# Optimization experiments

Hardware: AMD Instinct MI355X
Metric: run time of the kernel (lower is better)

The kernel has to match this reference:

```python
import jax, jax.numpy as jnp
import numpy as np

B, S, D = 2, 2048, 1024
H, KV, HD = 16, 4, 64
F, E, K = 2816, 8, 2
EPS = 1e-6

def setup_inputs() -> dict:
    key = jax.random.key(0)
    ks = jax.random.split(key, 9)
    def rn(k, shape, std=0.02):
        return jax.random.normal(k, shape, dtype=jnp.float32) * std
    inv_freq = 1.0 / (10000.0 ** (jnp.arange(0, HD, 2, dtype=jnp.float32) / HD))
    freqs = jnp.arange(S, dtype=jnp.float32)[:, None] * inv_freq[None, :]
    emb = jnp.concatenate([freqs, freqs], axis=-1)  # [S, HD]
    return {
        'hidden_states': rn(ks[0], (B, S, D), 1.0),
        'ln1_w': jnp.ones((D,), jnp.float32),
        'ln2_w': jnp.ones((D,), jnp.float32),
        'q_w': rn(ks[1], (H * HD, D)), 'q_b': jnp.zeros((H * HD,), jnp.float32),
        'k_w': rn(ks[2], (KV * HD, D)), 'k_b': jnp.zeros((KV * HD,), jnp.float32),
        'v_w': rn(ks[3], (KV * HD, D)), 'v_b': jnp.zeros((KV * HD,), jnp.float32),
        'o_w': rn(ks[4], (D, H * HD)),
        'router_w': rn(ks[5], (E, D), 0.01),
        'gate_w': rn(ks[6], (E, D, F)),
        'up_w': rn(ks[7], (E, D, F)),
        'down_w': rn(ks[8], (E, F, D)),
        'cos': jnp.cos(emb), 'sin': jnp.sin(emb),
    }

def _rmsnorm(x, w):
    v = jnp.mean(jnp.square(x.astype(jnp.float32)), axis=-1, keepdims=True)
    return (x.astype(jnp.float32) * jax.lax.rsqrt(v + EPS)).astype(x.dtype) * w

def _rotate_half(x):
    h = x.shape[-1] // 2
    return jnp.concatenate([-x[..., h:], x[..., :h]], axis=-1)

def reference(hidden_states, ln1_w, ln2_w, q_w, q_b, k_w, k_b, v_w, v_b, o_w, router_w, gate_w, up_w, down_w, cos, sin):
    # --- attention block (RMSNorm -> Qwen2Attention with RoPE+GQA -> residual) ---
    residual = hidden_states
    h = _rmsnorm(hidden_states, ln1_w)
    q = (h @ q_w.T + q_b).reshape(B, S, H, HD).transpose(0, 2, 1, 3)   # [B,H,S,HD]
    k = (h @ k_w.T + k_b).reshape(B, S, KV, HD).transpose(0, 2, 1, 3)  # [B,KV,S,HD]
    v = (h @ v_w.T + v_b).reshape(B, S, KV, HD).transpose(0, 2, 1, 3)
    c = cos[None, None]; s = sin[None, None]
    q = q * c + _rotate_half(q) * s
    k = k * c + _rotate_half(k) * s
    rep = H // KV
    k = jnp.repeat(k, rep, axis=1)
    v = jnp.repeat(v, rep, axis=1)
    scores = jnp.einsum('bhqd,bhkd->bhqk', q, k) / jnp.sqrt(jnp.float32(HD))
    causal = jnp.tril(jnp.ones((S, S), dtype=bool))
    scores = jnp.where(causal[None, None], scores, jnp.finfo(scores.dtype).min)
    attn = jax.nn.softmax(scores, axis=-1)
    ctx = jnp.einsum('bhqk,bhkd->bhqd', attn, v).transpose(0, 2, 1, 3).reshape(B, S, H * HD)
    x = ctx @ o_w.T + residual
    # --- MoE block (RMSNorm -> router -> expert SwiGLU MLPs -> combine -> residual) ---
    residual = x
    t = _rmsnorm(x, ln2_w).reshape(-1, D)  # [T, D], T = B*S
    logits = t @ router_w.T                # [T, E]
    probs = jax.nn.softmax(logits, axis=-1)
    topk_p, topk_i = jax.lax.top_k(probs, K)
    topk_p = topk_p / jnp.sum(topk_p, axis=-1, keepdims=True)
    # dispatch/combine weights [T,E]: vectorized form of the per-token scatter loop
    w = jnp.sum(jax.nn.one_hot(topk_i, E, dtype=t.dtype) * topk_p[..., None], axis=1)
    aux_loss = jnp.mean(E * jnp.square(jnp.mean(probs, axis=0)))
    out = jnp.zeros_like(t)
    for e in range(E):  # fixed small expert loop
        he = jax.nn.silu(t @ gate_w[e]) * (t @ up_w[e])
        out = out + (he @ down_w[e]) * w[:, e:e + 1]
    x = out.reshape(B, S, D) + residual
    return (x, aux_loss)
```

## Files before the change

### kernel.cpp

```cpp
#include <hip/hip_runtime.h>
#include <hip/hip_bf16.h>

#define DEVI __device__ __forceinline__

typedef float f32x4 __attribute__((ext_vector_type(4)));
typedef _Float16 f16x8 __attribute__((ext_vector_type(8)));
typedef short s16x8 __attribute__((ext_vector_type(8)));
typedef unsigned int u32;

constexpr int Bc = 2, Sc = 2048, Dc = 1024, Hc = 16, KVc = 4, HDc = 64, Fc = 2816, Ec = 8;
constexpr int Tc = Bc * Sc;
constexpr int QKVN = Hc * HDc + 2 * KVc * HDc;
constexpr int CAP = Tc * 2 + Ec * 128;
constexpr float LO_SCALE = 1024.0f;
constexpr float LO_INV = 1.0f / 1024.0f;

DEVI f32x4 mfma16(f16x8 a, f16x8 b, f32x4 c) {
    return __builtin_amdgcn_mfma_f32_16x16x32_f16(a, b, c, 0, 0, 0);
}
DEVI f32x4 mfma16(s16x8 a, s16x8 b, f32x4 c) {
    return __builtin_amdgcn_mfma_f32_16x16x32_bf16(a, b, c, 0, 0, 0);
}

DEVI void gll16(const void *g, void *l) {
    __builtin_amdgcn_global_load_lds(
        (const __attribute__((address_space(1))) u32 *)g,
        (__attribute__((address_space(3))) u32 *)l, 16, 0, 0);
}

DEVI u32 pack2(_Float16 a, _Float16 b) {
    union { _Float16 h[2]; u32 u; } t;
    t.h[0] = a; t.h[1] = b;
    return t.u;
}

template <int N> DEVI void wait_vm() {
    if constexpr (N == 0) asm volatile("s_waitcnt vmcnt(0)" ::: "memory");
    else if constexpr (N == 4) asm volatile("s_waitcnt vmcnt(4)" ::: "memory");
    else if constexpr (N == 6) asm volatile("s_waitcnt vmcnt(6)" ::: "memory");
    else if constexpr (N == 8) asm volatile("s_waitcnt vmcnt(8)" ::: "memory");
}

template <typename VT> struct FragT;
template <> struct FragT<_Float16> { using type = f16x8; };
template <> struct FragT<__hip_bfloat16> { using type = s16x8; };

struct GemmP {
    const void *Ah, *Al;
    const void *Bh, *Bl, *Bh2;
    long lda, ldb, bExp, K;
    const int *poff, *gidx;
    const float *bias, *resid, *bw;
    float *outF, *outF2;
    __hip_bfloat16 *outBF;
    _Float16 *rQh, *rQl, *rKh, *rKl;
    long ldc;
    int epi;
};

template <typename VT, bool SPLIT, bool GATHER, bool GU, int BN, bool XSWZ = false>
__global__ __launch_bounds__(256, SPLIT ? 3 : ((GU && BN == 128) ? 2 : 4)) void gemm_k(GemmP p) {
    constexpr int BM = 128;
    constexpr int NJ = BN / 32;
    constexpr bool HAS2 = SPLIT || GU;
    constexpr int ACH = SPLIT ? 1024 : 512;
    constexpr int BCH = BN * 4;
    constexpr int NB = HAS2 ? 2 : 1;
    constexpr int TOT = ACH + NB * BCH;
    constexpr int NCH = TOT / 256;
    constexpr int BUFVT = TOT * 8;
    constexpr int AOFF2 = 4096;
    constexpr int BOFF = ACH * 8;
    constexpr int B2OFF = (ACH + BCH) * 8;
    __shared__ __align__(16) VT s[2][BUFVT];
    const int tid = threadIdx.x, lane = tid & 63;
    const int wid = tid >> 6, wm = wid >> 1, wn = wid & 1;
    const int x = lane & 15, hi = lane >> 4;
    int mb = (int)blockIdx.x;
    if constexpr (XSWZ) mb = (mb & 7) * ((int)gridDim.x >> 3) + (mb >> 3);
    long m0 = (long)mb * BM, n0 = (long)blockIdx.y * BN;
    int e = 0;
    if (p.poff) {
        int tot = p.poff[Ec];
        if (m0 >= tot) return;
        while (m0 >= p.poff[e + 1]) ++e;
    }

    const VT *gs[NCH];
    int chd[NCH];
#pragma unroll
    for (int i = 0; i < NCH; ++i) {
        int ch = tid + i * 256;
        chd[i] = ch;
        if (ch < ACH) {
            int slab = ch >> 9, local = ch & 511;
            int r = local >> 2, c = local & 3;
            int cs = c ^ ((r >> 1) & 3);
            long ar = m0 + r;
            if (GATHER) ar = p.gidx[ar];
            const VT *mat = (SPLIT && slab == 1) ? (const VT *)p.Al : (const VT *)p.Ah;
            gs[i] = mat + ar * p.lda + cs * 8;
        } else {
            int idx = ch - ACH;
            int which = idx / BCH, local = idx % BCH;
            int r = local >> 2, c = local & 3;
            int cs = c ^ ((r >> 1) & 3);
            const VT *bmat = (which == 0) ? (const VT *)p.Bh
                           : (SPLIT ? (const VT *)p.Bl : (const VT *)p.Bh2);
            gs[i] = bmat + (long)e * p.bExp + (n0 + r) * p.ldb + cs * 8;
        }
    }

    f32x4 acc[4][NJ];
    f32x4 acc2[HAS2 ? 4 : 1][HAS2 ? NJ : 1];
#pragma unroll
    for (int i = 0; i < 4; ++i)
#pragma unroll
        for (int j = 0; j < NJ; ++j) {
            acc[i][j] = (f32x4){0.f, 0.f, 0.f, 0.f};
            if constexpr (HAS2) acc2[i][j] = (f32x4){0.f, 0.f, 0.f, 0.f};
        }

    using F8 = typename FragT<VT>::type;
    const int KT = (int)(p.K / 32);
    auto stageTo = [&](int kt, int b) {
#pragma unroll
        for (int i = 0; i < NCH; ++i)
            gll16(gs[i] + (long)kt * 32, &s[b][(size_t)chd[i] * 8]);
    };

    stageTo(0, 0);
    if (KT > 1) stageTo(1, 1);

    for (int kt = 0; kt < KT; ++kt) {
        if (kt + 1 < KT) wait_vm<NCH>();
        else wait_vm<0>();
        __builtin_amdgcn_sched_barrier(0);
        __builtin_amdgcn_s_barrier();
        __builtin_amdgcn_sched_barrier(0);
        const int cur = kt & 1;

        F8 afh[4], afl[SPLIT ? 4 : 1];
#pragma unroll
        for (int mi = 0; mi < 4; ++mi) {
            int ar = wm * 64 + mi * 16 + x;
            int ad = (ar * 4 + (hi ^ ((ar >> 1) & 3))) * 8;
            afh[mi] = *(const F8 *)&s[cur][ad];
            if constexpr (SPLIT) afl[mi] = *(const F8 *)&s[cur][AOFF2 + ad];
        }
        __builtin_amdgcn_s_setprio(1);
#pragma unroll
        for (int nj = 0; nj < NJ; ++nj) {
            int br = wn * (BN / 2) + nj * 16 + x;
            int bd = (br * 4 + (hi ^ ((br >> 1) & 3))) * 8;
            F8 bfh = *(const F8 *)&s[cur][BOFF + bd];
            F8 bf2;
            if constexpr (HAS2) bf2 = *(const F8 *)&s[cur][B2OFF + bd];
#pragma unroll
            for (int mi = 0; mi < 4; ++mi) {
                acc[mi][nj] = mfma16(afh[mi], bfh, acc[mi][nj]);
                if constexpr (SPLIT) {
                    acc2[mi][nj] = mfma16(afh[mi], bf2, acc2[mi][nj]);
                    acc2[mi][nj] = mfma16(afl[mi], bfh, acc2[mi][nj]);
                }
                if constexpr (GU) acc2[mi][nj] = mfma16(afh[mi], bf2, acc2[mi][nj]);
            }
        }
        __builtin_amdgcn_s_setprio(0);

        asm volatile("s_waitcnt lgkmcnt(0)" ::: "memory");
        __builtin_amdgcn_sched_barrier(0);
        __builtin_amdgcn_s_barrier();
        __builtin_amdgcn_sched_barrier(0);
        if (kt + 2 < KT) stageTo(kt + 2, cur);
    }

    if (SPLIT && p.epi == 6) {
        float *sEpi = (float *)&s[0][0];
#pragma unroll
        for (int mi = 0; mi < 4; ++mi)
#pragma unroll
            for (int nj = 0; nj < NJ; ++nj)
#pragma unroll
                for (int r = 0; r < 4; ++r) {
                    int rl = wm * 64 + mi * 16 + hi * 4 + r;
                    int cl = wn * (BN / 2) + nj * 16 + x;
                    float v = fmaf(acc2[mi][nj][r], LO_INV, acc[mi][nj][r]) + p.bias[n0 + cl];
                    sEpi[rl * 64 + cl] = v;
                }
        __syncthreads();
        const bool isV = (n0 >= 1280);
        const bool isK = (n0 >= 1024) && !isV;
#pragma unroll
        for (int mi = 0; mi < 4; ++mi)
#pragma unroll
            for (int nj = 0; nj < NJ; ++nj)
#pragma unroll
                for (int r = 0; r < 4; ++r) {
                    int rl = wm * 64 + mi * 16 + hi * 4 + r;
                    int cl = wn * (BN / 2) + nj * 16 + x;
                    long row = m0 + rl;
                    float xv = sEpi[rl * 64 + cl];
                    if (isV) {
                        p.outF[row * 256 + (n0 - 1280) + cl] = xv;
                    } else {
                        int spos = (int)(row & (Sc - 1));
                        float xp = sEpi[rl * 64 + (cl ^ 32)];
                        float cs = p.resid[spos * 64 + cl];
                        float sn = p.bw[spos * 64 + cl];
                        float o = xv * cs + ((cl < 32) ? -xp : xp) * sn;
                        _Float16 hv = (_Float16)o;
                        _Float16 lo = (_Float16)((o - (float)hv) * LO_SCALE);
                        if (isK) {
                            long off = row * 256 + (n0 - 1024) + cl;
                            p.rKh[off] = hv; p.rKl[off] = lo;
                        } else {
                            long off = row * 1024 + n0 + cl;
                            p.rQh[off] = hv; p.rQl[off] = lo;
                        }
                    }
                }
        return;
    }

#pragma unroll
    for (int mi = 0; mi < 4; ++mi)
#pragma unroll
        for (int nj = 0; nj < NJ; ++nj)
#pragma unroll
            for (int r = 0; r < 4; ++r) {
                long row = m0 + wm * 64 + mi * 16 + hi * 4 + r;
                long col = n0 + wn * (BN / 2) + nj * 16 + x;
                float v = acc[mi][nj][r];
                if constexpr (GU) {
                    float u = acc2[mi][nj][r];
                    float he = v / (1.f + __expf(-v)) * u;
                    p.outBF[row * p.ldc + col] = __float2bfloat16(he);
                } else {
                    if constexpr (SPLIT) v = fmaf(acc2[mi][nj][r], LO_INV, v);
                    switch (p.epi) {
                    case 0: p.outF[row * p.ldc + col] = v + p.bias[col]; break;
                    case 2: {
                        float o = v + p.resid[row * p.ldc + col];
                        p.outF[row * p.ldc + col] = o;
                        p.outF2[row * p.ldc + col] = o;
                    } break;
                    case 5:
                        p.outF[row * p.ldc + col] = v * p.bw[row];
                        break;
                    }
                }
            }
}

__global__ __launch_bounds__(256) void combine_k(const float *__restrict__ scat,
        const int *__restrict__ tok_slot, float *__restrict__ out) {
    const long tok = blockIdx.x;
    const int c = threadIdx.x * 4;
    const long s0 = tok_slot[tok * 2], s1 = tok_slot[tok * 2 + 1];
    f32x4 a = *(const f32x4 *)(scat + s0 * Dc + c);
    f32x4 b = *(const f32x4 *)(scat + s1 * Dc + c);
    f32x4 o = *(const f32x4 *)(out + tok * Dc + c);
#pragma unroll
    for (int j = 0; j < 4; ++j) o[j] += a[j] + b[j];
    *(f32x4 *)(out + tok * Dc + c) = o;
}

__global__ __launch_bounds__(128, 2) void attn_k(
    const _Float16 *__restrict__ qh, const _Float16 *__restrict__ ql,
    const _Float16 *__restrict__ kh, const _Float16 *__restrict__ kl,
    const _Float16 *__restrict__ vTh, const _Float16 *__restrict__ vTl,
    _Float16 *__restrict__ ctxh, _Float16 *__restrict__ ctxl) {
    __shared__ __align__(16) _Float16 kbuf[2][2][32 * 64];
    __shared__ __align__(16) _Float16 vbuf[2][2][64 * 32];
    const int tid = threadIdx.x, lane = tid & 63, wid = tid >> 6;
    const int x = lane & 15, hi = lane >> 4;
    const int pairI = blockIdx.x;
    const int bh = blockIdx.y;
    const int b = bh >> 4, h = bh & 15, kvh = h >> 2;
    const long kRow0 = (long)b * Sc * 256;
    const long vRow0 = (long)(b * 4 + kvh) * 64 * (long)Sc;

    auto stage = [&](int kt, int bufI) {
        if (wid == 0) {
#pragma unroll
            for (int ss = 0; ss < 2; ++ss) {
                const _Float16 *src = ss ? kl : kh;
#pragma unroll
                for (int i = 0; i < 4; ++i) {
                    int kv = 8 * i + (lane >> 3);
                    int cd = (lane & 7) ^ (kv & 7);
                    const _Float16 *g = src + kRow0 + ((long)kt * 32 + kv) * 256 + kvh * 64 + cd * 8;
                    gll16(g, &kbuf[bufI][ss][i * 512]);
                }
            }
        } else {
#pragma unroll
            for (int ss = 0; ss < 2; ++ss) {
                const _Float16 *src = ss ? vTl : vTh;
#pragma unroll
                for (int i = 0; i < 4; ++i) {
                    int d = 16 * i + (lane >> 2);
                    int ckv = (lane & 3) ^ ((d >> 1) & 3);
                    const _Float16 *g = src + vRow0 + (long)d * Sc + (long)kt * 32 + ckv * 8;
                    gll16(g, &vbuf[bufI][ss][i * 512]);
                }
            }
        }
    };

    for (int seg = 0; seg < 2; ++seg) {
        const int qt = seg ? (63 - pairI) : pairI;
        const int q0 = qt * 32;
        const long qtokW = (long)b * Sc + q0 + wid * 16;

        f16x8 qfh[2], qfl[2];
#pragma unroll
        for (int ks = 0; ks < 2; ++ks) {
            long off = (qtokW + x) * (long)Dc + h * 64 + ks * 32 + hi * 8;
            qfh[ks] = *(const f16x8 *)(qh + off);
            qfl[ks] = *(const f16x8 *)(ql + off);
        }
        asm volatile("s_waitcnt vmcnt(0)" ::: "memory");
        __builtin_amdgcn_sched_barrier(0);

        f32x4 o1[4], o2[4];
        float mrow = -3.0e38f, lrow = 0.f;
#pragma unroll
        for (int dj = 0; dj < 4; ++dj) {
            o1[dj] = (f32x4){0.f, 0.f, 0.f, 0.f};
            o2[dj] = (f32x4){0.f, 0.f, 0.f, 0.f};
        }

        const int NT = qt + 1;

        stage(0, 0);
        stage(1, 1);

        for (int kt = 0; kt < NT; ++kt) {
            if (kt + 1 < NT) asm volatile("s_waitcnt vmcnt(8)" ::: "memory");
            else asm volatile("s_waitcnt vmcnt(0)" ::: "memory");
            __builtin_amdgcn_sched_barrier(0);
            __builtin_amdgcn_s_barrier();
            __builtin_amdgcn_sched_barrier(0);
            const int cur = kt & 1;

            f32x4 s1[2], s2[2];
#pragma unroll
            for (int kvs = 0; kvs < 2; ++kvs) {
                s1[kvs] = (f32x4){0.f, 0.f, 0.f, 0.f};
                s2[kvs] = (f32x4){0.f, 0.f, 0.f, 0.f};
            }
            __builtin_amdgcn_s_setprio(1);
#pragma unroll
            for (int ks = 0; ks < 2; ++ks)
#pragma unroll
                for (int kvs = 0; kvs < 2; ++kvs) {
                    int row = kvs * 16 + x;
                    int addr = row * 64 + (((ks * 4 + hi) ^ (row & 7)) << 3);
                    f16x8 kfh = *(const f16x8 *)&kbuf[cur][0][addr];
                    f16x8 kfl = *(const f16x8 *)&kbuf[cur][1][addr];
                    s1[kvs] = mfma16(kfh, qfh[ks], s1[kvs]);
                    s2[kvs] = mfma16(kfl, qfh[ks], s2[kvs]);
                    s2[kvs] = mfma16(kfh, qfl[ks], s2[kvs]);
                }
            __builtin_amdgcn_s_setprio(0);

            const bool diag = (kt == NT - 1);
            const int qpos = q0 + wid * 16 + x;
            float sv[2][4];
#pragma unroll
            for (int kvs = 0; kvs < 2; ++kvs)
#pragma unroll
                for (int r = 0; r < 4; ++r) {
                    float v = fmaf(s2[kvs][r], LO_INV, s1[kvs][r]) * 0.125f;
                    if (diag) {
                        int kvpos = kt * 32 + kvs * 16 + 4 * hi + r;
                        if (kvpos > qpos) v = -3.0e38f;
                    }
                    sv[kvs][r] = v;
                }
            float mx = sv[0][0];
#pragma unroll
            for (int kvs = 0; kvs < 2; ++kvs)
#pragma unroll
                for (int r = 0; r < 4; ++r) mx = fmaxf(mx, sv[kvs][r]);
            mx = fmaxf(mx, __shfl_xor(mx, 16));
            mx = fmaxf(mx, __shfl_xor(mx, 32));
            if (!__all(mx - mrow <= 8.0f)) {
                float mnew = fmaxf(mrow, mx);
                float scl = __expf(mrow - mnew);
                mrow = mnew;
                lrow *= scl;
                float sclr[4];
#pragma unroll
                for (int r = 0; r < 4; ++r) sclr[r] = __shfl(scl, 4 * hi + r);
#pragma unroll
                for (int dj = 0; dj < 4; ++dj)
#pragma unroll
                    for (int r = 0; r < 4; ++r) {
                        o1[dj][r] *= sclr[r];
                        o2[dj][r] *= sclr[r];
                    }
            }
            float pv[2][4];
            float ls = 0.f;
#pragma unroll
            for (int kvs = 0; kvs < 2; ++kvs)
#pragma unroll
                for (int r = 0; r < 4; ++r) {
                    pv[kvs][r] = __expf(sv[kvs][r] - mrow);
                    ls += pv[kvs][r];
                }
            ls += __shfl_xor(ls, 16);
            ls += __shfl_xor(ls, 32);
            lrow += ls;
            u32 Bh0[2], Bh1[2], Bl0[2], Bl1[2];
#pragma unroll
            for (int pr = 0; pr < 2; ++pr) {
                _Float16 a0 = (_Float16)pv[0][2 * pr], a1 = (_Float16)pv[0][2 * pr + 1];
                _Float16 b0 = (_Float16)pv[1][2 * pr], b1 = (_Float16)pv[1][2 * pr + 1];
                Bh0[pr] = pack2(a0, a1);
                Bh1[pr] = pack2(b0, b1);
                _Float16 la0 = (_Float16)((pv[0][2 * pr] - (float)a0) * LO_SCALE);
                _Float16 la1 = (_Float16)((pv[0][2 * pr + 1] - (float)a1) * LO_SCALE);
                _Float16 lb0 = (_Float16)((pv[1][2 * pr] - (float)b0) * LO_SCALE);
                _Float16 lb1 = (_Float16)((pv[1][2 * pr + 1] - (float)b1) * LO_SCALE);
                Bl0[pr] = pack2(la0, la1);
                Bl1[pr] = pack2(lb0, lb1);
            }
            const int srcLow = x + ((lane & 16) ? 32 : 0);
            const int srcHigh = srcLow + 16;
            const bool useB1 = lane >= 32;
            union { u32 u[4]; f16x8 v; } fh, fl;
#pragma unroll
            for (int pr = 0; pr < 2; ++pr) {
                u32 t0 = (u32)__shfl((int)Bh0[pr], srcLow);
                u32 t1 = (u32)__shfl((int)Bh1[pr], srcLow);
                fh.u[pr] = useB1 ? t1 : t0;
                u32 u0 = (u32)__shfl((int)Bh0[pr], srcHigh);
                u32 u1 = (u32)__shfl((int)Bh1[pr], srcHigh);
                fh.u[2 + pr] = useB1 ? u1 : u0;
                u32 s0 = (u32)__shfl((int)Bl0[pr], srcLow);
                u32 s1v = (u32)__shfl((int)Bl1[pr], srcLow);
                fl.u[pr] = useB1 ? s1v : s0;
                u32 w0 = (u32)__shfl((int)Bl0[pr], srcHigh);
                u32 w1 = (u32)__shfl((int)Bl1[pr], srcHigh);
                fl.u[2 + pr] = useB1 ? w1 : w0;
            }
            f16x8 pah = fh.v, pal = fl.v;

            __builtin_amdgcn_s_setprio(1);
#pragma unroll
            for (int dj = 0; dj < 4; ++dj) {
                int d = dj * 16 + x;
                int addr = d * 32 + ((hi ^ ((d >> 1) & 3)) << 3);
                f16x8 vhf = *(const f16x8 *)&vbuf[cur][0][addr];
                f16x8 vlf = *(const f16x8 *)&vbuf[cur][1][addr];
                o1[dj] = mfma16(pah, vhf, o1[dj]);
                o2[dj] = mfma16(pah, vlf, o2[dj]);
                o2[dj] = mfma16(pal, vhf, o2[dj]);
            }
            __builtin_amdgcn_s_setprio(0);

            asm volatile("s_waitcnt lgkmcnt(0)" ::: "memory");
            __builtin_amdgcn_sched_barrier(0);
            __builtin_amdgcn_s_barrier();
            __builtin_amdgcn_sched_barrier(0);
            if (kt + 2 < NT) stage(kt + 2, cur);
        }

        float linv = 1.0f / lrow;
        float lr[4];
#pragma unroll
        for (int r = 0; r < 4; ++r) lr[r] = __shfl(linv, 4 * hi + r);
#pragma unroll
        for (int dj = 0; dj < 4; ++dj)
#pragma unroll
            for (int r = 0; r < 4; ++r) {
                long tok = qtokW + 4 * hi + r;
                float ov = fmaf(o2[dj][r], LO_INV, o1[dj][r]) * lr[r];
                _Float16 hv = (_Float16)ov;
                long off = tok * Dc + h * 64 + dj * 16 + x;
                ctxh[off] = hv;
                ctxl[off] = (_Float16)((ov - (float)hv) * LO_SCALE);
            }
    }
}

__global__ __launch_bounds__(256) void rmsnorm_split_k(const float *__restrict__ x,
        const float *__restrict__ w, _Float16 *__restrict__ oh, _Float16 *__restrict__ ol) {
    const long row = blockIdx.x;
    const int tid = threadIdx.x, lane = tid & 63, wid = tid >> 6;
    f32x4 v = *(const f32x4 *)(x + row * Dc + tid * 4);
    float ss = v[0] * v[0] + v[1] * v[1] + v[2] * v[2] + v[3] * v[3];
#pragma unroll
    for (int off = 1; off < 64; off <<= 1) ss += __shfl_xor(ss, off);
    __shared__ float sw[4];
    if (lane == 0) sw[wid] = ss;
    __syncthreads();
    float inv = 1.0f / sqrtf((sw[0] + sw[1] + sw[2] + sw[3]) * (1.f / Dc) + 1e-6f);
#pragma unroll
    for (int j = 0; j < 4; ++j) {
        float y = v[j] * inv * w[tid * 4 + j];
        _Float16 hv = (_Float16)y;
        oh[row * Dc + tid * 4 + j] = hv;
        ol[row * Dc + tid * 4 + j] = (_Float16)((y - (float)hv) * LO_SCALE);
    }
}

__global__ __launch_bounds__(256) void rmsnorm2_k(const float *__restrict__ x,
        const float *__restrict__ w, float *__restrict__ tf, __hip_bfloat16 *__restrict__ tb) {
    const long row = blockIdx.x;
    const int tid = threadIdx.x, lane = tid & 63, wid = tid >> 6;
    f32x4 v = *(const f32x4 *)(x + row * Dc + tid * 4);
    float ss = v[0] * v[0] + v[1] * v[1] + v[2] * v[2] + v[3] * v[3];
#pragma unroll
    for (int off = 1; off < 64; off <<= 1) ss += __shfl_xor(ss, off);
    __shared__ float sw[4];
    if (lane == 0) sw[wid] = ss;
    __syncthreads();
    float inv = 1.0f / sqrtf((sw[0] + sw[1] + sw[2] + sw[3]) * (1.f / Dc) + 1e-6f);
#pragma unroll
    for (int j = 0; j < 4; ++j) {
        float y = v[j] * inv * w[tid * 4 + j];
        tf[row * Dc + tid * 4 + j] = y;
        tb[row * Dc + tid * 4 + j] = __float2bfloat16(y);
    }
}

__global__ void split_f16_k(const float *__restrict__ x, _Float16 *hi, _Float16 *lo, long n) {
    for (long i = (long)blockIdx.x * 256 + threadIdx.x; i < n; i += (long)gridDim.x * 256) {
        float v = x[i];
        _Float16 h = (_Float16)v;
        hi[i] = h;
        lo[i] = (_Float16)((v - (float)h) * LO_SCALE);
    }
}

__global__ void pack_qkvw_k(const float *__restrict__ qw, const float *__restrict__ kw,
        const float *__restrict__ vw, _Float16 *wh, _Float16 *wl) {
    const long n = (long)QKVN * Dc;
    for (long i = (long)blockIdx.x * 256 + threadIdx.x; i < n; i += (long)gridDim.x * 256) {
        long o = i >> 10;
        int d = (int)(i & 1023);
        float v;
        if (o < 1024) v = qw[o * 1024 + d];
        else if (o < 1280) v = kw[(o - 1024) * 1024 + d];
        else v = vw[(o - 1280) * 1024 + d];
        _Float16 h = (_Float16)v;
        wh[i] = h;
        wl[i] = (_Float16)((v - (float)h) * LO_SCALE);
    }
}

__global__ void pack_bias_k(const float *qb, const float *kb, const float *vb, float *out) {
    int i = blockIdx.x * 256 + threadIdx.x;
    if (i >= QKVN) return;
    out[i] = (i < 1024) ? qb[i] : (i < 1280) ? kb[i - 1024] : vb[i - 1280];
}

__global__ __launch_bounds__(256) void transpose_bf16_k(const float *__restrict__ in,
        __hip_bfloat16 *__restrict__ out, int R, int C) {
    __shared__ float tile[64 * 65];
    const long eo = (long)blockIdx.z * R * C;
    const int r0 = blockIdx.y * 64, c0 = blockIdx.x * 64;
#pragma unroll
    for (int i = 0; i < 16; ++i) {
        int idx = threadIdx.x + i * 256;
        int r = idx >> 6, c = idx & 63;
        tile[r * 65 + c] = in[eo + (long)(r0 + r) * C + (c0 + c)];
    }
    __syncthreads();
#pragma unroll
    for (int i = 0; i < 16; ++i) {
        int idx = threadIdx.x + i * 256;
        int cc = idx >> 6, rr = idx & 63;
        out[eo + (long)(c0 + cc) * R + (r0 + rr)] = __float2bfloat16(tile[rr * 65 + cc]);
    }
}

__global__ __launch_bounds__(256) void vtrans_k(const float *__restrict__ vqf,
        _Float16 *__restrict__ vTh, _Float16 *__restrict__ vTl) {
    __shared__ float tile[64][65];
    const int tok0 = blockIdx.x * 64;
    const int bk = blockIdx.y;
    const int b = bk >> 2, kvh = bk & 3;
#pragma unroll
    for (int it = 0; it < 16; ++it) {
        int idx = it * 256 + threadIdx.x;
        int r = idx >> 6, c = idx & 63;
        tile[r][c] = vqf[((long)b * Sc + tok0 + r) * 256 + kvh * 64 + c];
    }
    __syncthreads();
    const int d = threadIdx.x & 63, ch = threadIdx.x >> 6;
    long orow = ((long)bk * 64 + d) * (long)Sc + tok0 + ch * 16;
    f16x8 oh[2], ol[2];
#pragma unroll
    for (int j = 0; j < 16; ++j) {
        float v = tile[ch * 16 + j][d];
        _Float16 hv = (_Float16)v;
        oh[j >> 3][j & 7] = hv;
        ol[j >> 3][j & 7] = (_Float16)((v - (float)hv) * LO_SCALE);
    }
    *(f16x8 *)(vTh + orow) = oh[0];
    *(f16x8 *)(vTh + orow + 8) = oh[1];
    *(f16x8 *)(vTl + orow) = ol[0];
    *(f16x8 *)(vTl + orow + 8) = ol[1];
}

__global__ __launch_bounds__(256) void router_p1_k(const float *__restrict__ t,
        const float *__restrict__ rw, float *probs, int *tok_e, float *tok_w, int *cnt) {
    const int tid = threadIdx.x, lane = tid & 63, wid = tid >> 6;
    const long tok = (long)blockIdx.x * 4 + wid;
    const float *row = t + tok * Dc;
    const int d0 = lane * 16;
    f32x4 xv[4];
#pragma unroll
    for (int i = 0; i < 4; ++i) xv[i] = *(const f32x4 *)(row + d0 + i * 4);
    float acc[8];
#pragma unroll
    for (int e = 0; e < 8; ++e) {
        const float *wr = rw + (long)e * Dc + d0;
        float a = 0.f;
#pragma unroll
        for (int i = 0; i < 4; ++i) {
            f32x4 wv = *(const f32x4 *)(wr + i * 4);
            a += xv[i][0] * wv[0] + xv[i][1] * wv[1] + xv[i][2] * wv[2] + xv[i][3] * wv[3];
        }
        acc[e] = a;
    }
#pragma unroll
    for (int off = 1; off < 64; off <<= 1)
#pragma unroll
        for (int e = 0; e < 8; ++e) acc[e] += __shfl_xor(acc[e], off);
    if (lane == 0) {
        float mx = acc[0];
#pragma unroll
        for (int e = 1; e < 8; ++e) mx = fmaxf(mx, acc[e]);
        float ex[8], s = 0.f;
#pragma unroll
        for (int e = 0; e < 8; ++e) { ex[e] = expf(acc[e] - mx); s += ex[e]; }
        float inv = 1.f / s;
        int i1 = -1, i2 = -1;
        float p1v = -1.f, p2v = -1.f;
#pragma unroll
        for (int e = 0; e < 8; ++e) {
            float pe = ex[e] * inv;
            probs[tok * 8 + e] = pe;
            if (pe > p1v) { i2 = i1; p2v = p1v; i1 = e; p1v = pe; }
            else if (pe > p2v) { i2 = e; p2v = pe; }
        }
        float wsum = p1v + p2v;
        tok_e[tok * 2] = i1; tok_e[tok * 2 + 1] = i2;
        tok_w[tok * 2] = p1v / wsum; tok_w[tok * 2 + 1] = p2v / wsum;
        atomicAdd(&cnt[i1], 1);
        atomicAdd(&cnt[i2], 1);
    }
}

__global__ __launch_bounds__(1024) void router_p2_k(const int *cnt, const float *probs,
        int *poff, float *aux_out) {
    __shared__ float sd[1024];
    const int tid = threadIdx.x;
    const int e = tid & 7, rs = tid >> 3;
    float s = 0.f;
    for (int r = rs; r < Tc; r += 128) s += probs[(long)r * 8 + e];
    sd[tid] = s;
    __syncthreads();
    for (int st = 64; st >= 1; st >>= 1) {
        if (rs < st) sd[tid] += sd[tid + st * 8];
        __syncthreads();
    }
    if (tid == 0) {
        float a = 0.f;
        for (int ee = 0; ee < 8; ++ee) {
            float m = sd[ee] * (1.f / Tc);
            a += m * m;
        }
        aux_out[0] = a;
        int o = 0;
        poff[0] = 0;
        for (int ee = 0; ee < 8; ++ee) { o += (cnt[ee] + 127) & ~127; poff[ee + 1] = o; }
    }
}

__global__ void router_p3_k(const int *tok_e, const float *tok_w, const int *poff,
        int *cursor, int *btok, float *bw, int *tok_slot) {
    long tok = (long)blockIdx.x * 256 + threadIdx.x;
    if (tok >= Tc) return;
#pragma unroll
    for (int j = 0; j < 2; ++j) {
        int e = tok_e[tok * 2 + j];
        int slot = atomicAdd(&cursor[e], 1);
        btok[poff[e] + slot] = (int)tok;
        bw[poff[e] + slot] = tok_w[tok * 2 + j];
        tok_slot[tok * 2 + j] = poff[e] + slot;
    }
}

__global__ void router_p4_k(const int *poff, const int *cnt, int *btok, float *bw) {
    int s = blockIdx.x * 256 + threadIdx.x;
    if (s >= poff[8]) return;
    int e = 0;
    while (s >= poff[e + 1]) ++e;
    if (s - poff[e] >= cnt[e]) { btok[s] = 0; bw[s] = 0.f; }
}

extern "C" void kernel_launch(void *const *d_in, const int *in_sizes, int n_in,
                              void *d_out, int out_size, void *d_ws, size_t ws_size,
                              hipStream_t stream) {
    (void)in_sizes; (void)n_in;
    const float *hidden = (const float *)d_in[0];
    const float *ln1 = (const float *)d_in[1];
    const float *ln2 = (const float *)d_in[2];
    const float *qw = (const float *)d_in[3];
    const float *qb = (const float *)d_in[4];
    const float *kw = (const float *)d_in[5];
    const float *kb = (const float *)d_in[6];
    const float *vw = (const float *)d_in[7];
    const float *vb = (const float *)d_in[8];
    const float *ow = (const float *)d_in[9];
    const float *rw = (const float *)d_in[10];
    const float *gw = (const float *)d_in[11];
    const float *uw = (const float *)d_in[12];
    const float *dwn = (const float *)d_in[13];
    const float *cosb = (const float *)d_in[14];
    const float *sinb = (const float *)d_in[15];
    float *outx = (float *)d_out;

    char *base = (char *)d_ws;
    size_t off = 0;
    auto alloc = [&](size_t bytes) -> char * {
        char *p = base + off;
        off += (bytes + 255) & ~(size_t)255;
        return p;
    };
    _Float16 *qkvwh = (_Float16 *)alloc((size_t)QKVN * Dc * 2);
    _Float16 *qkvwl = (_Float16 *)alloc((size_t)QKVN * Dc * 2);
    float *qkvb = (float *)alloc(QKVN * 4);
    _Float16 *owh = (_Float16 *)alloc((size_t)Dc * Dc * 2);
    _Float16 *owl = (_Float16 *)alloc((size_t)Dc * Dc * 2);
    __hip_bfloat16 *gateT = (__hip_bfloat16 *)alloc((size_t)Ec * Fc * Dc * 2);
    __hip_bfloat16 *upT = (__hip_bfloat16 *)alloc((size_t)Ec * Fc * Dc * 2);
    __hip_bfloat16 *downT = (__hip_bfloat16 *)alloc((size_t)Ec * Dc * Fc * 2);
    char *U2 = alloc((size_t)Tc * Dc * 4);
    _Float16 *hh = (_Float16 *)U2;
    _Float16 *hl = hh + (size_t)Tc * Dc;
    float *tf = (float *)U2;
    char *U3 = alloc((size_t)Tc * Dc * 4);
    _Float16 *qhb = (_Float16 *)U3;
    _Float16 *qlb = qhb + (size_t)Tc * Dc;
    float *x1 = (float *)U3;
    _Float16 *khb = (_Float16 *)alloc((size_t)Tc * 256 * 2);
    _Float16 *klb = (_Float16 *)alloc((size_t)Tc * 256 * 2);
    _Float16 *vTh = (_Float16 *)alloc((size_t)Tc * 256 * 2);
    _Float16 *vTl = (_Float16 *)alloc((size_t)Tc * 256 * 2);
    float *scat = (float *)U2;
    _Float16 *ctxh = (_Float16 *)alloc((size_t)Tc * Dc * 2);
    _Float16 *ctxl = (_Float16 *)alloc((size_t)Tc * Dc * 2);
    __hip_bfloat16 *tbf = (__hip_bfloat16 *)alloc((size_t)Tc * Dc * 2);
    float *vqf = (float *)alloc((size_t)Tc * 256 * 4);
    float *probs = (float *)alloc((size_t)Tc * 8 * 4);
    int *tok_e = (int *)alloc((size_t)Tc * 2 * 4);
    float *tok_w = (float *)alloc((size_t)Tc * 2 * 4);
    int *tok_slot = (int *)alloc((size_t)Tc * 2 * 4);
    int *cnt = (int *)alloc(256);
    int *cursor = cnt + 8;
    int *poff = (int *)alloc(256);
    int *btok = (int *)alloc((size_t)CAP * 4);
    float *bwgt = (float *)alloc((size_t)CAP * 4);
    __hip_bfloat16 *gbuf = (__hip_bfloat16 *)alloc((size_t)CAP * Fc * 2);

    if (off > ws_size) {
        hipMemsetAsync(d_out, 0, (size_t)out_size * 4, stream);
        return;
    }

    hipMemsetAsync(cnt, 0, 64, stream);
    pack_qkvw_k<<<1024, 256, 0, stream>>>(qw, kw, vw, qkvwh, qkvwl);
    pack_bias_k<<<(QKVN + 255) / 256, 256, 0, stream>>>(qb, kb, vb, qkvb);
    split_f16_k<<<1024, 256, 0, stream>>>(ow, owh, owl, (long)Dc * Dc);
    transpose_bf16_k<<<dim3(Fc / 64, Dc / 64, Ec), 256, 0, stream>>>(gw, gateT, Dc, Fc);
    transpose_bf16_k<<<dim3(Fc / 64, Dc / 64, Ec), 256, 0, stream>>>(uw, upT, Dc, Fc);
    transpose_bf16_k<<<dim3(Dc / 64, Fc / 64, Ec), 256, 0, stream>>>(dwn, downT, Fc, Dc);
    rmsnorm_split_k<<<Tc, 256, 0, stream>>>(hidden, ln1, hh, hl);

    GemmP g{};
    g.Ah = hh; g.Al = hl; g.Bh = qkvwh; g.Bl = qkvwl;
    g.lda = Dc; g.ldb = Dc; g.bExp = 0; g.K = Dc;
    g.bias = qkvb; g.resid = cosb; g.bw = sinb;
    g.outF = vqf; g.rQh = qhb; g.rQl = qlb; g.rKh = khb; g.rKl = klb;
    g.ldc = QKVN; g.epi = 6;
    gemm_k<_Float16, true, false, false, 64><<<dim3(Tc / 128, QKVN / 64), 256, 0, stream>>>(g);

    vtrans_k<<<dim3(Sc / 64, Bc * KVc), 256, 0, stream>>>(vqf, vTh, vTl);
    attn_k<<<dim3(Sc / 64, Bc * Hc), 128, 0, stream>>>(qhb, qlb, khb, klb, vTh, vTl, ctxh, ctxl);

    GemmP go{};
    go.Ah = ctxh; go.Al = ctxl; go.Bh = owh; go.Bl = owl;
    go.lda = Dc; go.ldb = Dc; go.bExp = 0; go.K = Dc;
    go.resid = hidden; go.outF = x1; go.outF2 = outx; go.ldc = Dc; go.epi = 2;
    gemm_k<_Float16, true, false, false, 64><<<dim3(Tc / 128, Dc / 64), 256, 0, stream>>>(go);

    rmsnorm2_k<<<Tc, 256, 0, stream>>>(x1, ln2, tf, tbf);
    router_p1_k<<<Tc / 4, 256, 0, stream>>>(tf, rw, probs, tok_e, tok_w, cnt);
    router_p2_k<<<1, 1024, 0, stream>>>(cnt, probs, poff, outx + (long)Tc * Dc);
    router_p3_k<<<Tc / 256, 256, 0, stream>>>(tok_e, tok_w, poff, cursor, btok, bwgt, tok_slot);
    router_p4_k<<<CAP / 256, 256, 0, stream>>>(poff, cnt, btok, bwgt);

    GemmP gg{};
    gg.Ah = tbf; gg.Bh = gateT; gg.Bh2 = upT;
    gg.lda = Dc; gg.ldb = Dc; gg.bExp = (long)Fc * Dc; gg.K = Dc;
    gg.poff = poff; gg.gidx = btok; gg.outBF = gbuf; gg.ldc = Fc;
    gemm_k<__hip_bfloat16, false, true, true, 128, true><<<dim3(CAP / 128, Fc / 128), 256, 0, stream>>>(gg);

    GemmP gd{};
    gd.Ah = gbuf; gd.Bh = downT;
    gd.lda = Fc; gd.ldb = Fc; gd.bExp = (long)Dc * Fc; gd.K = Fc;
    gd.poff = poff; gd.bw = bwgt;
    gd.outF = scat; gd.ldc = Dc; gd.epi = 5;
    gemm_k<__hip_bfloat16, false, false, false, 128, true><<<dim3(CAP / 128, Dc / 128), 256, 0, stream>>>(gd);

    combine_k<<<Tc, 256, 0, stream>>>(scat, tok_slot, outx);
}
```

Before: 693.3 us.

## Triple-buffer MoE GEMM staging and fuse RMSNorm with router kernel

Adds a configurable number of LDS stage buffers to the GEMM template and uses three buffers for the gate/up and down expert GEMMs. This deepens the global-to-LDS prefetch pipeline, with vmcnt waits adjusted to match. It also fuses the second RMSNorm with the router logits/softmax/top-k into one kernel, which removes the fp32 normalized-activation write and re-read. Risks: the extra LDS per block can lower occupancy, especially for the gate/up GEMM, whose launch bounds already allow only 2 blocks per unit.

```diff
diff --git a/kernel.cpp b/kernel.cpp
--- a/kernel.cpp
+++ b/kernel.cpp
@@ -39,6 +39,7 @@
     else if constexpr (N == 4) asm volatile("s_waitcnt vmcnt(4)" ::: "memory");
     else if constexpr (N == 6) asm volatile("s_waitcnt vmcnt(6)" ::: "memory");
     else if constexpr (N == 8) asm volatile("s_waitcnt vmcnt(8)" ::: "memory");
+    else if constexpr (N == 12) asm volatile("s_waitcnt vmcnt(12)" ::: "memory");
 }
 
 template <typename VT> struct FragT;
@@ -58,7 +59,7 @@
     int epi;
 };
 
-template <typename VT, bool SPLIT, bool GATHER, bool GU, int BN, bool XSWZ = false>
+template <typename VT, bool SPLIT, bool GATHER, bool GU, int BN, bool XSWZ = false, int NBUF = 2>
 __global__ __launch_bounds__(256, SPLIT ? 3 : ((GU && BN == 128) ? 2 : 4)) void gemm_k(GemmP p) {
     constexpr int BM = 128;
     constexpr int NJ = BN / 32;
@@ -72,7 +73,7 @@
     constexpr int AOFF2 = 4096;
     constexpr int BOFF = ACH * 8;
     constexpr int B2OFF = (ACH + BCH) * 8;
-    __shared__ __align__(16) VT s[2][BUFVT];
+    __shared__ __align__(16) VT s[NBUF][BUFVT];
     const int tid = threadIdx.x, lane = tid & 63;
     const int wid = tid >> 6, wm = wid >> 1, wn = wid & 1;
     const int x = lane & 15, hi = lane >> 4;
@@ -130,15 +131,18 @@
     };
 
     stageTo(0, 0);
-    if (KT > 1) stageTo(1, 1);
-
+    if (KT > 1) stageTo(1, 1 % NBUF);
+    if (NBUF == 3 && KT > 2) stageTo(2, 2 % NBUF);
+
+    int cur = 0;
     for (int kt = 0; kt < KT; ++kt) {
-        if (kt + 1 < KT) wait_vm<NCH>();
+        const int rem = KT - 1 - kt;
+        if (rem >= NBUF - 1) wait_vm<(NBUF - 1) * NCH>();
+        else if (NBUF == 3 && rem == 1) wait_vm<NCH>();
         else wait_vm<0>();
         __builtin_amdgcn_sched_barrier(0);
         __builtin_amdgcn_s_barrier();
         __builtin_amdgcn_sched_barrier(0);
-        const int cur = kt & 1;
 
         F8 afh[4], afl[SPLIT ? 4 : 1];
 #pragma unroll
@@ -172,7 +176,8 @@
         __builtin_amdgcn_sched_barrier(0);
         __builtin_amdgcn_s_barrier();
         __builtin_amdgcn_sched_barrier(0);
-        if (kt + 2 < KT) stageTo(kt + 2, cur);
+        if (kt + NBUF < KT) stageTo(kt + NBUF, cur);
+        cur = (cur + 1 == NBUF) ? 0 : cur + 1;
     }
 
     if (SPLIT && p.epi == 6) {
@@ -509,8 +514,10 @@
     }
 }
 
-__global__ __launch_bounds__(256) void rmsnorm2_k(const float *__restrict__ x,
-        const float *__restrict__ w, float *__restrict__ tf, __hip_bfloat16 *__restrict__ tb) {
+__global__ __launch_bounds__(256) void rmsnorm_router_k(const float *__restrict__ x,
+        const float *__restrict__ w, const float *__restrict__ rw,
+        __hip_bfloat16 *__restrict__ tb, float *__restrict__ probs,
+        int *__restrict__ tok_e, float *__restrict__ tok_w, int *__restrict__ cnt) {
     const long row = blockIdx.x;
     const int tid = threadIdx.x, lane = tid & 63, wid = tid >> 6;
     f32x4 v = *(const f32x4 *)(x + row * Dc + tid * 4);
@@ -518,23 +525,56 @@
 #pragma unroll
     for (int off = 1; off < 64; off <<= 1) ss += __shfl_xor(ss, off);
     __shared__ float sw[4];
+    __shared__ float part[4][8];
     if (lane == 0) sw[wid] = ss;
     __syncthreads();
     float inv = 1.0f / sqrtf((sw[0] + sw[1] + sw[2] + sw[3]) * (1.f / Dc) + 1e-6f);
+    float y[4];
 #pragma unroll
     for (int j = 0; j < 4; ++j) {
-        float y = v[j] * inv * w[tid * 4 + j];
-        tf[row * Dc + tid * 4 + j] = y;
-        tb[row * Dc + tid * 4 + j] = __float2bfloat16(y);
-    }
-}
-
-__global__ void split_f16_k(const float *__restrict__ x, _Float16 *hi, _Float16 *lo, long n) {
-    for (long i = (long)blockIdx.x * 256 + threadIdx.x; i < n; i += (long)gridDim.x * 256) {
-        float v = x[i];
-        _Float16 h = (_Float16)v;
-        hi[i] = h;
-        lo[i] = (_Float16)((v - (float)h) * LO_SCALE);
+        y[j] = v[j] * inv * w[tid * 4 + j];
+        tb[row * Dc + tid * 4 + j] = __float2bfloat16(y[j]);
+    }
+    float acc[8];
+#pragma unroll
+    for (int e = 0; e < 8; ++e) {
+        f32x4 wv = *(const f32x4 *)(rw + (long)e * Dc + tid * 4);
+        acc[e] = y[0] * wv[0] + y[1] * wv[1] + y[2] * wv[2] + y[3] * wv[3];
+    }
+#pragma unroll
+    for (int off = 1; off < 64; off <<= 1)
+#pragma unroll
+        for (int e = 0; e < 8; ++e) acc[e] += __shfl_xor(acc[e], off);
+    if (lane == 0)
+#pragma unroll
+        for (int e = 0; e < 8; ++e) part[wid][e] = acc[e];
+    __syncthreads();
+    if (tid == 0) {
+        float lg[8];
+        float mx = -3.0e38f;
+#pragma unroll
+        for (int e = 0; e < 8; ++e) {
+            lg[e] = part[0][e] + part[1][e] + part[2][e] + part[3][e];
+            mx = fmaxf(mx, lg[e]);
+        }
+        float ex[8], s = 0.f;
+#pragma unroll
+        for (int e = 0; e < 8; ++e) { ex[e] = expf(lg[e] - mx); s += ex[e]; }
+        float invs = 1.f / s;
+        int i1 = -1, i2 = -1;
+        float p1v = -1.f, p2v = -1.f;
+#pragma unroll
+        for (int e = 0; e < 8; ++e) {
+            float pe = ex[e] * invs;
+            probs[row * 8 + e] = pe;
+            if (pe > p1v) { i2 = i1; p2v = p1v; i1 = e; p1v = pe; }
+            else if (pe > p2v) { i2 = e; p2v = pe; }
+        }
+        float wsum = p1v + p2v;
+        tok_e[row * 2] = i1; tok_e[row * 2 + 1] = i2;
+        tok_w[row * 2] = p1v / wsum; tok_w[row * 2 + 1] = p2v / wsum;
+        atomicAdd(&cnt[i1], 1);
+        atomicAdd(&cnt[i2], 1);
     }
 }
 
@@ -554,6 +594,15 @@
     }
 }
 
+__global__ void split_f16_k(const float *__restrict__ x, _Float16 *hi, _Float16 *lo, long n) {
+    for (long i = (long)blockIdx.x * 256 + threadIdx.x; i < n; i += (long)gridDim.x * 256) {
+        float v = x[i];
+        _Float16 h = (_Float16)v;
+        hi[i] = h;
+        lo[i] = (_Float16)((v - (float)h) * LO_SCALE);
+    }
+}
+
 __global__ void pack_bias_k(const float *qb, const float *kb, const float *vb, float *out) {
     int i = blockIdx.x * 256 + threadIdx.x;
     if (i >= QKVN) return;
@@ -607,56 +656,6 @@
     *(f16x8 *)(vTh + orow + 8) = oh[1];
     *(f16x8 *)(vTl + orow) = ol[0];
     *(f16x8 *)(vTl + orow + 8) = ol[1];
-}
-
-__global__ __launch_bounds__(256) void router_p1_k(const float *__restrict__ t,
-        const float *__restrict__ rw, float *probs, int *tok_e, float *tok_w, int *cnt) {
-    const int tid = threadIdx.x, lane = tid & 63, wid = tid >> 6;
-    const long tok = (long)blockIdx.x * 4 + wid;
-    const float *row = t + tok * Dc;
-    const int d0 = lane * 16;
-    f32x4 xv[4];
-#pragma unroll
-    for (int i = 0; i < 4; ++i) xv[i] = *(const f32x4 *)(row + d0 + i * 4);
-    float acc[8];
-#pragma unroll
-    for (int e = 0; e < 8; ++e) {
-        const float *wr = rw + (long)e * Dc + d0;
-        float a = 0.f;
-#pragma unroll
-        for (int i = 0; i < 4; ++i) {
-            f32x4 wv = *(const f32x4 *)(wr + i * 4);
-            a += xv[i][0] * wv[0] + xv[i][1] * wv[1] + xv[i][2] * wv[2] + xv[i][3] * wv[3];
-        }
-        acc[e] = a;
-    }
-#pragma unroll
-    for (int off = 1; off < 64; off <<= 1)
-#pragma unroll
-        for (int e = 0; e < 8; ++e) acc[e] += __shfl_xor(acc[e], off);
-    if (lane == 0) {
-        float mx = acc[0];
-#pragma unroll
-        for (int e = 1; e < 8; ++e) mx = fmaxf(mx, acc[e]);
-        float ex[8], s = 0.f;
-#pragma unroll
-        for (int e = 0; e < 8; ++e) { ex[e] = expf(acc[e] - mx); s += ex[e]; }
-        float inv = 1.f / s;
-        int i1 = -1, i2 = -1;
-        float p1v = -1.f, p2v = -1.f;
-#pragma unroll
-        for (int e = 0; e < 8; ++e) {
-            float pe = ex[e] * inv;
-            probs[tok * 8 + e] = pe;
-            if (pe > p1v) { i2 = i1; p2v = p1v; i1 = e; p1v = pe; }
-            else if (pe > p2v) { i2 = e; p2v = pe; }
-        }
-        float wsum = p1v + p2v;
-        tok_e[tok * 2] = i1; tok_e[tok * 2 + 1] = i2;
-        tok_w[tok * 2] = p1v / wsum; tok_w[tok * 2 + 1] = p2v / wsum;
-        atomicAdd(&cnt[i1], 1);
-        atomicAdd(&cnt[i2], 1);
-    }
 }
 
 __global__ __launch_bounds__(1024) void router_p2_k(const int *cnt, const float *probs,
@@ -747,7 +746,6 @@
     char *U2 = alloc((size_t)Tc * Dc * 4);
     _Float16 *hh = (_Float16 *)U2;
     _Float16 *hl = hh + (size_t)Tc * Dc;
-    float *tf = (float *)U2;
     char *U3 = alloc((size_t)Tc * Dc * 4);
     _Float16 *qhb = (_Float16 *)U3;
     _Float16 *qlb = qhb + (size_t)Tc * Dc;
@@ -803,8 +801,7 @@
     go.resid = hidden; go.outF = x1; go.outF2 = outx; go.ldc = Dc; go.epi = 2;
     gemm_k<_Float16, true, false, false, 64><<<dim3(Tc / 128, Dc / 64), 256, 0, stream>>>(go);
 
-    rmsnorm2_k<<<Tc, 256, 0, stream>>>(x1, ln2, tf, tbf);
-    router_p1_k<<<Tc / 4, 256, 0, stream>>>(tf, rw, probs, tok_e, tok_w, cnt);
+    rmsnorm_router_k<<<Tc, 256, 0, stream>>>(x1, ln2, rw, tbf, probs, tok_e, tok_w, cnt);
     router_p2_k<<<1, 1024, 0, stream>>>(cnt, probs, poff, outx + (long)Tc * Dc);
     router_p3_k<<<Tc / 256, 256, 0, stream>>>(tok_e, tok_w, poff, cursor, btok, bwgt, tok_slot);
     router_p4_k<<<CAP / 256, 256, 0, stream>>>(poff, cnt, btok, bwgt);
@@ -813,14 +810,14 @@
     gg.Ah = tbf; gg.Bh = gateT; gg.Bh2 = upT;
     gg.lda = Dc; gg.ldb = Dc; gg.bExp = (long)Fc * Dc; gg.K = Dc;
     gg.poff = poff; gg.gidx = btok; gg.outBF = gbuf; gg.ldc = Fc;
-    gemm_k<__hip_bfloat16, false, true, true, 128, true><<<dim3(CAP / 128, Fc / 128), 256, 0, stream>>>(gg);
+    gemm_k<__hip_bfloat16, false, true, true, 128, true, 3><<<dim3(CAP / 128, Fc / 128), 256, 0, stream>>>(gg);
 
     GemmP gd{};
     gd.Ah = gbuf; gd.Bh = downT;
     gd.lda = Fc; gd.ldb = Fc; gd.bExp = (long)Dc * Fc; gd.K = Fc;
     gd.poff = poff; gd.bw = bwgt;
     gd.outF = scat; gd.ldc = Dc; gd.epi = 5;
-    gemm_k<__hip_bfloat16, false, false, false, 128, true><<<dim3(CAP / 128, Dc / 128), 256, 0, stream>>>(gd);
+    gemm_k<__hip_bfloat16, false, false, false, 128, true, 3><<<dim3(CAP / 128, Dc / 128), 256, 0, stream>>>(gd);
 
     combine_k<<<Tc, 256, 0, stream>>>(scat, tok_slot, outx);
 }
```

After: 680.9 us. No clear change (-1.8%).
